# Kernel tuning notes

Measured on AMD Instinct MI355X. Metric: run time of the kernel, lower is better.

## Reference

```python
import jax, jax.numpy as jnp
import numpy as np

IN_SIZE = 768
FC_SIZE = 3072
H = 12
ATT = IN_SIZE // H
EPS = 1e-5


def setup_inputs() -> dict:
    key = jax.random.key(0)
    ks = jax.random.split(key, 12)
    B, S = 4, 1024
    x = jax.random.normal(ks[0], (B, S, IN_SIZE), dtype=jnp.float32)
    mask = jax.random.randint(ks[1], (B, S, S), 0, 2, dtype=jnp.int32)
    s = 1.0 / np.sqrt(IN_SIZE)
    WQ = jax.random.normal(ks[2], (IN_SIZE, IN_SIZE), dtype=jnp.float32) * s
    WK = jax.random.normal(ks[3], (IN_SIZE, IN_SIZE), dtype=jnp.float32) * s
    WV = jax.random.normal(ks[4], (IN_SIZE, IN_SIZE), dtype=jnp.float32) * s
    Wfc = jax.random.normal(ks[5], (IN_SIZE, IN_SIZE), dtype=jnp.float32) * s
    W1 = jax.random.normal(ks[6], (IN_SIZE, FC_SIZE), dtype=jnp.float32) * s
    b1 = jnp.zeros((FC_SIZE,), dtype=jnp.float32)
    W2 = jax.random.normal(ks[7], (FC_SIZE, IN_SIZE), dtype=jnp.float32) / np.sqrt(FC_SIZE)
    b2 = jnp.zeros((IN_SIZE,), dtype=jnp.float32)
    g1 = jnp.ones((IN_SIZE,), dtype=jnp.float32)
    be1 = jnp.zeros((IN_SIZE,), dtype=jnp.float32)
    g2 = jnp.ones((IN_SIZE,), dtype=jnp.float32)
    be2 = jnp.zeros((IN_SIZE,), dtype=jnp.float32)
    return dict(x=x, mask=mask, WQ=WQ, WK=WK, WV=WV, Wfc=Wfc,
                W1=W1, b1=b1, W2=W2, b2=b2, g1=g1, be1=be1, g2=g2, be2=be2)


def _layernorm(x, g, b):
    mu = jnp.mean(x, axis=-1, keepdims=True)
    var = jnp.var(x, axis=-1, keepdims=True)
    return (x - mu) * jax.lax.rsqrt(var + EPS) * g + b


def reference(x, mask, WQ, WK, WV, Wfc, W1, b1, W2, b2, g1, be1, g2, be2):
    B, S, D = x.shape
    # NOTE: original code scales by sqrt(h), not sqrt(head_dim)
    scale = np.sqrt(H).astype(np.float32)
    Q = (x @ WQ).reshape(B, S, H, ATT).transpose(0, 2, 1, 3)  # [B,H,S,d]
    K = (x @ WK).reshape(B, S, H, ATT).transpose(0, 2, 1, 3)
    V = (x @ WV).reshape(B, S, H, ATT).transpose(0, 2, 1, 3)
    alpha = jnp.einsum('bhqd,bhkd->bhqk', Q, K) / scale
    alpha = jnp.where(mask[:, None, :, :] == 0, -1e9, alpha)
    alpha = jax.nn.softmax(alpha, axis=-1)
    att = jnp.einsum('bhqk,bhkd->bhqd', alpha, V)
    att = att.transpose(0, 2, 1, 3).reshape(B, S, D)
    att = att @ Wfc
    norm_att = _layernorm(att + x, g1, be1)
    lin = jax.nn.relu(norm_att @ W1 + b1) @ W2 + b2
    out = _layernorm(lin + norm_att, g2, be2)
    return out
```

## Files before the change

### kernel.cpp

```cpp
#include <hip/hip_runtime.h>
#include <stdint.h>

#define DMODEL 768
#define DFC    3072
#define NHEAD  12
#define DHEAD  64
#define BSZ    4
#define SEQ    1024
#define NTOK   (BSZ*SEQ)
#define QKVN   (3*DMODEL)

typedef unsigned short u16;
typedef unsigned int   u32;
typedef unsigned long long u64;
typedef __bf16 bf16_t;
typedef bf16_t bf16x8 __attribute__((ext_vector_type(8)));
typedef float  f32x4  __attribute__((ext_vector_type(4)));

__device__ __forceinline__ u16 f2b(float f) {
  u32 u = __builtin_bit_cast(u32, f);
  u = (u + 0x7FFFu + ((u >> 16) & 1u)) >> 16;
  return (u16)u;
}

__device__ __forceinline__ void gload_lds16(const void* g, void* l) {
  __builtin_amdgcn_global_load_lds(
      (const __attribute__((address_space(1))) void*)g,
      (__attribute__((address_space(3))) void*)l, 16, 0, 0);
}


__global__ __launch_bounds__(256) void cast_f32_bf16(const float* __restrict__ in,
                                                     u16* __restrict__ out, int n4) {
  int i = blockIdx.x * 256 + threadIdx.x;
  if (i >= n4) return;
  float4 v = ((const float4*)in)[i];
  ushort4 o;
  o.x = f2b(v.x); o.y = f2b(v.y); o.z = f2b(v.z); o.w = f2b(v.w);
  ((ushort4*)out)[i] = o;
}

__global__ __launch_bounds__(256) void transpose_cast(const float* __restrict__ in,
                                                      u16* __restrict__ out, int K, int N) {
  __shared__ float tile[32][33];
  int bx = blockIdx.x * 32;
  int by = blockIdx.y * 32;
  int tx = threadIdx.x, ty = threadIdx.y;
#pragma unroll
  for (int i = 0; i < 4; ++i)
    tile[ty + i*8][tx] = in[(size_t)(by + ty + i*8) * N + bx + tx];
  __syncthreads();
#pragma unroll
  for (int i = 0; i < 4; ++i)
    out[(size_t)(bx + ty + i*8) * K + by + tx] = f2b(tile[tx][ty + i*8]);
}

__global__ __launch_bounds__(256) void pack_mask(const int* __restrict__ mask,
                                                 u64* __restrict__ mp) {
  int w = threadIdx.x >> 6, lane = threadIdx.x & 63;
  int idx = blockIdx.x * 4 + w;
  u64 bal = __ballot(mask[(size_t)idx * 64 + lane] != 0);
  if (lane == 0) mp[idx] = bal;
}

__global__ __launch_bounds__(256) void build_vt(const u16* __restrict__ QKVM,
                                                u16* __restrict__ VT) {
  __shared__ u16 t[64][72];
  int st = blockIdx.x, h = blockIdx.y, b = blockIdx.z;
  int tid = threadIdx.x;
  const u16* src = QKVM + ((size_t)(b * SEQ + st * 64)) * QKVN + 2 * DMODEL + h * DHEAD;
#pragma unroll
  for (int p = 0; p < 2; ++p) {
    int s = (p * 256 + tid) >> 3, c8 = tid & 7;
    *(uint4*)&t[s][c8 * 8] = *(const uint4*)&src[(size_t)s * QKVN + c8 * 8];
  }
  __syncthreads();
  u16* dst = VT + ((size_t)(b * NHEAD + h) * 64) * SEQ + st * 64;
#pragma unroll
  for (int p = 0; p < 2; ++p) {
    int d = (p * 256 + tid) >> 3, s8 = tid & 7;
    union { uint4 v; u16 s[8]; } o;
#pragma unroll
    for (int j = 0; j < 8; ++j) o.s[j] = t[s8 * 8 + j][d];
    *(uint4*)&dst[(size_t)d * SEQ + s8 * 8] = o.v;
  }
}

template <int MODE>
__global__ __launch_bounds__(256) void gemm_bt(const u16* __restrict__ A,
                                               const u16* __restrict__ Bt,
                                               void* __restrict__ Cout,
                                               const float* __restrict__ bias,
                                               int M, int N, int K) {
  __shared__ __align__(16) u16 ldsA[2][128 * 32];
  __shared__ __align__(16) u16 ldsB[2][128 * 32];
  int tid = threadIdx.x;
  int lane = tid & 63, l15 = lane & 15, g = lane >> 4;
  int w = tid >> 6, wm = w >> 1, wn = w & 1;
  int m0 = blockIdx.y * 128, n0 = blockIdx.x * 128;
  int NT = K >> 5;

  f32x4 acc[4][4];
#pragma unroll
  for (int i = 0; i < 4; ++i)
#pragma unroll
    for (int j = 0; j < 4; ++j) acc[i][j] = (f32x4){0.f, 0.f, 0.f, 0.f};

  const u16* gabase = A + (size_t)m0 * K;
  const u16* gbbase = Bt + (size_t)n0 * K;
  int wbase = tid & ~63;

  auto stage = [&](int kt, int buf) {
#pragma unroll
    for (int p = 0; p < 2; ++p) {
      int c = p * 256 + tid;
      int row = c >> 2, slot = c & 3;
      size_t goff = (size_t)row * K + kt * 32 + slot * 8;
      gload_lds16(gabase + goff, &ldsA[buf][(p * 256 + wbase) * 8]);
      gload_lds16(gbbase + goff, &ldsB[buf][(p * 256 + wbase) * 8]);
    }
  };

  stage(0, 0);
  __syncthreads();
  for (int kt = 0; kt < NT; ++kt) {
    int cur = kt & 1;
    if (kt + 1 < NT) stage(kt + 1, cur ^ 1);
    bf16x8 af[4], bfr[4];
#pragma unroll
    for (int i = 0; i < 4; ++i) {
      af[i]  = *(const bf16x8*)&ldsA[cur][(wm * 64 + i * 16 + l15) * 32 + g * 8];
      bfr[i] = *(const bf16x8*)&ldsB[cur][(wn * 64 + i * 16 + l15) * 32 + g * 8];
    }
#pragma unroll
    for (int i = 0; i < 4; ++i)
#pragma unroll
      for (int j = 0; j < 4; ++j)
        acc[i][j] = __builtin_amdgcn_mfma_f32_16x16x32_bf16(af[i], bfr[j], acc[i][j], 0, 0, 0);
    __syncthreads();
  }

#pragma unroll
  for (int i = 0; i < 4; ++i) {
#pragma unroll
    for (int j = 0; j < 4; ++j) {
#pragma unroll
      for (int r = 0; r < 4; ++r) {
        int row = m0 + wm * 64 + i * 16 + g * 4 + r;
        int col = n0 + wn * 64 + j * 16 + l15;
        float v = acc[i][j][r];
        if (MODE == 2 || MODE == 3) v += bias[col];
        if (MODE == 2) v = v > 0.f ? v : 0.f;
        if (MODE == 0 || MODE == 2)
          ((u16*)Cout)[(size_t)row * N + col] = f2b(v);
        else
          ((float*)Cout)[(size_t)row * N + col] = v;
      }
    }
  }
}

__global__ __launch_bounds__(256) void attn_kernel(const u16* __restrict__ QKVM,
                                                   const u16* __restrict__ VT,
                                                   const u64* __restrict__ MP,
                                                   u16* __restrict__ Om) {
  __shared__ __align__(16) u16 ldsK[2][64 * 64];
  __shared__ __align__(16) u16 ldsV[2][64 * 64];
  __shared__ __align__(16) u16 P_lds[4][16][72];

  int qt = blockIdx.x, h = blockIdx.y, b = blockIdx.z;
  int tid = threadIdx.x, w = tid >> 6, lane = tid & 63;
  int l15 = lane & 15, g = lane >> 4, l7 = lane & 7;
  int q0 = qt * 64 + w * 16;

  const u16* Qb = QKVM + (size_t)(b * SEQ) * QKVN + h * DHEAD;
  const u16* Kb = QKVM + (size_t)(b * SEQ) * QKVN + DMODEL + h * DHEAD;
  const u16* Vb = VT + (size_t)(b * NHEAD + h) * 64 * SEQ;

  bf16x8 qf[2];
  qf[0] = *(const bf16x8*)&Qb[(size_t)(q0 + l15) * QKVN + g * 8];
  qf[1] = *(const bf16x8*)&Qb[(size_t)(q0 + l15) * QKVN + 32 + g * 8];

  int r8 = lane >> 3, sl = lane & 7, slg = sl ^ r8;

  auto stage = [&](int kt, int buf) {
#pragma unroll
    for (int p = 0; p < 2; ++p) {
      int c = p * 4 + w;
      int row = c * 8 + r8;
      gload_lds16(Kb + (size_t)(kt * 64 + row) * QKVN + slg * 8, &ldsK[buf][c * 512]);
      gload_lds16(Vb + (size_t)row * SEQ + kt * 64 + slg * 8, &ldsV[buf][c * 512]);
    }
  };

  f32x4 acc[4];
  float ps[4];
#pragma unroll
  for (int d = 0; d < 4; ++d) acc[d] = (f32x4){0.f, 0.f, 0.f, 0.f};
#pragma unroll
  for (int r = 0; r < 4; ++r) ps[r] = 0.f;

  const float SC2 = 0.41650835f;

  stage(0, 0);
  __syncthreads();

  for (int kt = 0; kt < SEQ / 64; ++kt) {
    int cur = kt & 1;
    if (kt + 1 < SEQ / 64) stage(kt + 1, cur ^ 1);

    u64 mw[4];
#pragma unroll
    for (int r = 0; r < 4; ++r)
      mw[r] = MP[((size_t)(b * SEQ + q0 + g * 4 + r) << 4) | kt];

    f32x4 s[4];
#pragma unroll
    for (int fn = 0; fn < 4; ++fn) s[fn] = (f32x4){0.f, 0.f, 0.f, 0.f};
#pragma unroll
    for (int kf = 0; kf < 2; ++kf)
#pragma unroll
      for (int fn = 0; fn < 4; ++fn) {
        bf16x8 kfrag = *(const bf16x8*)((const char*)&ldsK[cur][0] +
                         (fn * 16 + l15) * 128 + (((kf * 4 + g) ^ l7) << 4));
        s[fn] = __builtin_amdgcn_mfma_f32_16x16x32_bf16(qf[kf], kfrag, s[fn], 0, 0, 0);
      }

#pragma unroll
    for (int fn = 0; fn < 4; ++fn) {
      u32 half0 = (fn & 2) ? (u32)(mw[0] >> 32) : (u32)mw[0];
      u32 half1 = (fn & 2) ? (u32)(mw[1] >> 32) : (u32)mw[1];
      u32 half2 = (fn & 2) ? (u32)(mw[2] >> 32) : (u32)mw[2];
      u32 half3 = (fn & 2) ? (u32)(mw[3] >> 32) : (u32)mw[3];
      u32 bitpos = ((fn & 1) << 4) + l15;
      u32 hv[4] = {half0, half1, half2, half3};
#pragma unroll
      for (int r = 0; r < 4; ++r) {
        float pe = __builtin_amdgcn_exp2f(s[fn][r] * SC2);
        float p = ((hv[r] >> bitpos) & 1u) ? pe : 0.f;
        ps[r] += p;
        P_lds[w][g * 4 + r][fn * 16 + l15] = f2b(p);
      }
    }

#pragma unroll
    for (int kf2 = 0; kf2 < 2; ++kf2) {
      bf16x8 pf = *(const bf16x8*)((const char*)&P_lds[w][0][0] +
                    l15 * 144 + (kf2 * 32 + g * 8) * 2);
#pragma unroll
      for (int d = 0; d < 4; ++d) {
        bf16x8 vf = *(const bf16x8*)((const char*)&ldsV[cur][0] +
                      (d * 16 + l15) * 128 + (((kf2 * 4 + g) ^ l7) << 4));
        acc[d] = __builtin_amdgcn_mfma_f32_16x16x32_bf16(pf, vf, acc[d], 0, 0, 0);
      }
    }
    __syncthreads();
  }

#pragma unroll
  for (int r = 0; r < 4; ++r) {
#pragma unroll
    for (int off = 1; off < 16; off <<= 1) ps[r] += __shfl_xor(ps[r], off);
    ps[r] = 1.f / ps[r];
  }
#pragma unroll
  for (int d = 0; d < 4; ++d)
#pragma unroll
    for (int r = 0; r < 4; ++r) {
      float o = acc[d][r] * ps[r];
      Om[(size_t)(b * SEQ + q0 + g * 4 + r) * DMODEL + h * DHEAD + d * 16 + l15] = f2b(o);
    }
}

template <bool WRITE_B16>
__global__ __launch_bounds__(256) void ln_res(const float* __restrict__ a,
                                              const float* __restrict__ res,
                                              const float* __restrict__ gam,
                                              const float* __restrict__ bet,
                                              float* __restrict__ of,
                                              u16* __restrict__ ob) {
  int w = threadIdx.x >> 6, lane = threadIdx.x & 63;
  int row = blockIdx.x * 4 + w;
  const float* pa = a + (size_t)row * DMODEL;
  const float* pr = res + (size_t)row * DMODEL;
  float v[12];
  float s = 0.f, s2 = 0.f;
#pragma unroll
  for (int j = 0; j < 12; ++j) {
    float x = pa[lane + j * 64] + pr[lane + j * 64];
    v[j] = x; s += x; s2 += x * x;
  }
#pragma unroll
  for (int off = 32; off; off >>= 1) {
    s += __shfl_xor(s, off);
    s2 += __shfl_xor(s2, off);
  }
  float mu = s * (1.f / DMODEL);
  float var = s2 * (1.f / DMODEL) - mu * mu;
  float rs = rsqrtf(var + 1e-5f);
#pragma unroll
  for (int j = 0; j < 12; ++j) {
    int c = lane + j * 64;
    float o = (v[j] - mu) * rs * gam[c] + bet[c];
    of[(size_t)row * DMODEL + c] = o;
    if (WRITE_B16) ob[(size_t)row * DMODEL + c] = f2b(o);
  }
}

extern "C" void kernel_launch(void* const* d_in, const int* in_sizes, int n_in,
                              void* d_out, int out_size, void* d_ws, size_t ws_size,
                              hipStream_t stream) {
  const float* x   = (const float*)d_in[0];
  const int*   msk = (const int*)d_in[1];
  const float* WQ  = (const float*)d_in[2];
  const float* WK  = (const float*)d_in[3];
  const float* WV  = (const float*)d_in[4];
  const float* Wfc = (const float*)d_in[5];
  const float* W1  = (const float*)d_in[6];
  const float* b1  = (const float*)d_in[7];
  const float* W2  = (const float*)d_in[8];
  const float* b2  = (const float*)d_in[9];
  const float* g1  = (const float*)d_in[10];
  const float* be1 = (const float*)d_in[11];
  const float* g2  = (const float*)d_in[12];
  const float* be2 = (const float*)d_in[13];
  float* out = (float*)d_out;

  char* ws = (char*)d_ws;
  size_t off = 0;
  auto alloc = [&](size_t bytes) {
    void* p = ws + off;
    off += (bytes + 255) & ~(size_t)255;
    return p;
  };
  u16* XB    = (u16*)alloc((size_t)NTOK * DMODEL * 2);
  u16* WQKVT = (u16*)alloc((size_t)QKVN * DMODEL * 2);
  u16* WFCT  = (u16*)alloc((size_t)DMODEL * DMODEL * 2);
  u16* W1T   = (u16*)alloc((size_t)DMODEL * DFC * 2);
  u16* W2T   = (u16*)alloc((size_t)DFC * DMODEL * 2);
  u16* QKVM  = (u16*)alloc((size_t)NTOK * QKVN * 2);
  u16* VT    = (u16*)alloc((size_t)NTOK * DMODEL * 2);
  u64* MP    = (u64*)alloc((size_t)BSZ * SEQ * (SEQ / 64) * 8);
  float* ATTP = (float*)alloc((size_t)NTOK * DMODEL * 4);
  float* NAF  = (float*)alloc((size_t)NTOK * DMODEL * 4);
  u16*  NAB   = (u16*)alloc((size_t)NTOK * DMODEL * 2);
  u16*  ATTO = XB;
  u16*  HMID = QKVM;
  float* LIN = ATTP;

  cast_f32_bf16<<<dim3((NTOK * DMODEL) / 4 / 256), dim3(256), 0, stream>>>(x, XB, (NTOK * DMODEL) / 4);
  transpose_cast<<<dim3(DMODEL / 32, DMODEL / 32), dim3(32, 8), 0, stream>>>(WQ, WQKVT, DMODEL, DMODEL);
  transpose_cast<<<dim3(DMODEL / 32, DMODEL / 32), dim3(32, 8), 0, stream>>>(WK, WQKVT + (size_t)DMODEL * DMODEL, DMODEL, DMODEL);
  transpose_cast<<<dim3(DMODEL / 32, DMODEL / 32), dim3(32, 8), 0, stream>>>(WV, WQKVT + (size_t)2 * DMODEL * DMODEL, DMODEL, DMODEL);
  transpose_cast<<<dim3(DMODEL / 32, DMODEL / 32), dim3(32, 8), 0, stream>>>(Wfc, WFCT, DMODEL, DMODEL);
  transpose_cast<<<dim3(DFC / 32, DMODEL / 32), dim3(32, 8), 0, stream>>>(W1, W1T, DMODEL, DFC);
  transpose_cast<<<dim3(DMODEL / 32, DFC / 32), dim3(32, 8), 0, stream>>>(W2, W2T, DFC, DMODEL);
  pack_mask<<<dim3(BSZ * SEQ * (SEQ / 64) / 4), dim3(256), 0, stream>>>(msk, MP);

  gemm_bt<0><<<dim3(QKVN / 128, NTOK / 128), dim3(256), 0, stream>>>(XB, WQKVT, QKVM, nullptr, NTOK, QKVN, DMODEL);
  build_vt<<<dim3(SEQ / 64, NHEAD, BSZ), dim3(256), 0, stream>>>(QKVM, VT);
  attn_kernel<<<dim3(SEQ / 64, NHEAD, BSZ), dim3(256), 0, stream>>>(QKVM, VT, MP, ATTO);

  gemm_bt<1><<<dim3(DMODEL / 128, NTOK / 128), dim3(256), 0, stream>>>(ATTO, WFCT, ATTP, nullptr, NTOK, DMODEL, DMODEL);
  ln_res<true><<<dim3(NTOK / 4), dim3(256), 0, stream>>>(ATTP, x, g1, be1, NAF, NAB);
  gemm_bt<2><<<dim3(DFC / 128, NTOK / 128), dim3(256), 0, stream>>>(NAB, W1T, HMID, b1, NTOK, DFC, DMODEL);
  gemm_bt<3><<<dim3(DMODEL / 128, NTOK / 128), dim3(256), 0, stream>>>(HMID, W2T, LIN, b2, NTOK, DMODEL, DFC);
  ln_res<false><<<dim3(NTOK / 4), dim3(256), 0, stream>>>(LIN, NAF, g2, be2, out, nullptr);

  (void)in_sizes; (void)n_in; (void)out_size; (void)ws_size;
}
```

Baseline: 327.9 us.

## Split-K the N=768 GEMMs with atomics and swizzle GEMM LDS layout

The two GEMMs with N=768 (output projection and second FFN matmul) now use split-K across blockIdx.z (2 and 4 ways) and accumulate into memset-zeroed fp32 buffers with atomicAdd. The b2 bias add moves into the final layernorm. The GEMM LDS staging and fragment reads get an XOR swizzle on the 16-byte slot to cut bank conflicts. Buffers are reassigned to fixed workspace offsets, and the fp32 accumulators alias QKVM and XB. The aim is more blocks for the small-grid GEMMs, at the cost of two memsets, atomic traffic, and a non-deterministic summation order.

```diff
diff --git a/kernel.cpp b/kernel.cpp
--- a/kernel.cpp
+++ b/kernel.cpp
@@ -86,7 +86,7 @@
   }
 }
 
-template <int MODE>
+template <int MODE, int SPLIT>
 __global__ __launch_bounds__(256) void gemm_bt(const u16* __restrict__ A,
                                                const u16* __restrict__ Bt,
                                                void* __restrict__ Cout,
@@ -98,7 +98,9 @@
   int lane = tid & 63, l15 = lane & 15, g = lane >> 4;
   int w = tid >> 6, wm = w >> 1, wn = w & 1;
   int m0 = blockIdx.y * 128, n0 = blockIdx.x * 128;
-  int NT = K >> 5;
+  int KS = K / SPLIT;
+  int k0 = blockIdx.z * KS;
+  int NT = KS >> 5;
 
   f32x4 acc[4][4];
 #pragma unroll
@@ -106,20 +108,23 @@
 #pragma unroll
     for (int j = 0; j < 4; ++j) acc[i][j] = (f32x4){0.f, 0.f, 0.f, 0.f};
 
-  const u16* gabase = A + (size_t)m0 * K;
-  const u16* gbbase = Bt + (size_t)n0 * K;
+  const u16* gabase = A + (size_t)m0 * K + k0;
+  const u16* gbbase = Bt + (size_t)n0 * K + k0;
   int wbase = tid & ~63;
+  int lswz = (lane & 3) ^ ((lane >> 3) & 3);
 
   auto stage = [&](int kt, int buf) {
 #pragma unroll
     for (int p = 0; p < 2; ++p) {
       int c = p * 256 + tid;
-      int row = c >> 2, slot = c & 3;
-      size_t goff = (size_t)row * K + kt * 32 + slot * 8;
+      int row = c >> 2;
+      size_t goff = (size_t)row * K + kt * 32 + lswz * 8;
       gload_lds16(gabase + goff, &ldsA[buf][(p * 256 + wbase) * 8]);
       gload_lds16(gbbase + goff, &ldsB[buf][(p * 256 + wbase) * 8]);
     }
   };
+
+  int rswz = (l15 >> 1) & 3;
 
   stage(0, 0);
   __syncthreads();
@@ -129,8 +134,8 @@
     bf16x8 af[4], bfr[4];
 #pragma unroll
     for (int i = 0; i < 4; ++i) {
-      af[i]  = *(const bf16x8*)&ldsA[cur][(wm * 64 + i * 16 + l15) * 32 + g * 8];
-      bfr[i] = *(const bf16x8*)&ldsB[cur][(wn * 64 + i * 16 + l15) * 32 + g * 8];
+      af[i]  = *(const bf16x8*)&ldsA[cur][(wm * 64 + i * 16 + l15) * 32 + (g ^ rswz) * 8];
+      bfr[i] = *(const bf16x8*)&ldsB[cur][(wn * 64 + i * 16 + l15) * 32 + (g ^ rswz) * 8];
     }
 #pragma unroll
     for (int i = 0; i < 4; ++i)
@@ -149,12 +154,14 @@
         int row = m0 + wm * 64 + i * 16 + g * 4 + r;
         int col = n0 + wn * 64 + j * 16 + l15;
         float v = acc[i][j][r];
-        if (MODE == 2 || MODE == 3) v += bias[col];
-        if (MODE == 2) v = v > 0.f ? v : 0.f;
-        if (MODE == 0 || MODE == 2)
+        if (MODE == 2) {
+          v += bias[col];
+          v = v > 0.f ? v : 0.f;
+        }
+        if (MODE == 4)
+          atomicAdd(&((float*)Cout)[(size_t)row * N + col], v);
+        else
           ((u16*)Cout)[(size_t)row * N + col] = f2b(v);
-        else
-          ((float*)Cout)[(size_t)row * N + col] = v;
       }
     }
   }
@@ -228,12 +235,11 @@
 
 #pragma unroll
     for (int fn = 0; fn < 4; ++fn) {
-      u32 half0 = (fn & 2) ? (u32)(mw[0] >> 32) : (u32)mw[0];
-      u32 half1 = (fn & 2) ? (u32)(mw[1] >> 32) : (u32)mw[1];
-      u32 half2 = (fn & 2) ? (u32)(mw[2] >> 32) : (u32)mw[2];
-      u32 half3 = (fn & 2) ? (u32)(mw[3] >> 32) : (u32)mw[3];
+      u32 hv[4];
+#pragma unroll
+      for (int r = 0; r < 4; ++r)
+        hv[r] = (fn & 2) ? (u32)(mw[r] >> 32) : (u32)mw[r];
       u32 bitpos = ((fn & 1) << 4) + l15;
-      u32 hv[4] = {half0, half1, half2, half3};
 #pragma unroll
       for (int r = 0; r < 4; ++r) {
         float pe = __builtin_amdgcn_exp2f(s[fn][r] * SC2);
@@ -272,9 +278,10 @@
     }
 }
 
-template <bool WRITE_B16>
+template <bool WRITE_B16, bool ADDB>
 __global__ __launch_bounds__(256) void ln_res(const float* __restrict__ a,
                                               const float* __restrict__ res,
+                                              const float* __restrict__ badd,
                                               const float* __restrict__ gam,
                                               const float* __restrict__ bet,
                                               float* __restrict__ of,
@@ -287,7 +294,9 @@
   float s = 0.f, s2 = 0.f;
 #pragma unroll
   for (int j = 0; j < 12; ++j) {
-    float x = pa[lane + j * 64] + pr[lane + j * 64];
+    int c = lane + j * 64;
+    float x = pa[c] + pr[c];
+    if (ADDB) x += badd[c];
     v[j] = x; s += x; s2 += x * x;
   }
 #pragma unroll
@@ -327,26 +336,20 @@
   float* out = (float*)d_out;
 
   char* ws = (char*)d_ws;
-  size_t off = 0;
-  auto alloc = [&](size_t bytes) {
-    void* p = ws + off;
-    off += (bytes + 255) & ~(size_t)255;
-    return p;
-  };
-  u16* XB    = (u16*)alloc((size_t)NTOK * DMODEL * 2);
-  u16* WQKVT = (u16*)alloc((size_t)QKVN * DMODEL * 2);
-  u16* WFCT  = (u16*)alloc((size_t)DMODEL * DMODEL * 2);
-  u16* W1T   = (u16*)alloc((size_t)DMODEL * DFC * 2);
-  u16* W2T   = (u16*)alloc((size_t)DFC * DMODEL * 2);
-  u16* QKVM  = (u16*)alloc((size_t)NTOK * QKVN * 2);
-  u16* VT    = (u16*)alloc((size_t)NTOK * DMODEL * 2);
-  u64* MP    = (u64*)alloc((size_t)BSZ * SEQ * (SEQ / 64) * 8);
-  float* ATTP = (float*)alloc((size_t)NTOK * DMODEL * 4);
-  float* NAF  = (float*)alloc((size_t)NTOK * DMODEL * 4);
-  u16*  NAB   = (u16*)alloc((size_t)NTOK * DMODEL * 2);
-  u16*  ATTO = XB;
-  u16*  HMID = QKVM;
-  float* LIN = ATTP;
+  u16*  XB    = (u16*)(ws + 0);
+  u16*  WQKVT = (u16*)(ws + 6291456);
+  u16*  WFCT  = (u16*)(ws + 9830400);
+  u16*  W1T   = (u16*)(ws + 11010048);
+  u16*  W2T   = (u16*)(ws + 15728640);
+  u16*  QKVM  = (u16*)(ws + 20447232);
+  u16*  VT    = (u16*)(ws + 39321600);
+  u64*  MP    = (u64*)(ws + 45613056);
+  float* NAF  = (float*)(ws + 46137344);
+  u16*  NAB   = (u16*)(ws + 58720256);
+  u16*   ATTO    = XB;
+  float* PROJACC = (float*)QKVM;
+  u16*   HMID    = QKVM;
+  float* LINACC  = (float*)ws;
 
   cast_f32_bf16<<<dim3((NTOK * DMODEL) / 4 / 256), dim3(256), 0, stream>>>(x, XB, (NTOK * DMODEL) / 4);
   transpose_cast<<<dim3(DMODEL / 32, DMODEL / 32), dim3(32, 8), 0, stream>>>(WQ, WQKVT, DMODEL, DMODEL);
@@ -357,15 +360,18 @@
   transpose_cast<<<dim3(DMODEL / 32, DFC / 32), dim3(32, 8), 0, stream>>>(W2, W2T, DFC, DMODEL);
   pack_mask<<<dim3(BSZ * SEQ * (SEQ / 64) / 4), dim3(256), 0, stream>>>(msk, MP);
 
-  gemm_bt<0><<<dim3(QKVN / 128, NTOK / 128), dim3(256), 0, stream>>>(XB, WQKVT, QKVM, nullptr, NTOK, QKVN, DMODEL);
+  gemm_bt<0, 1><<<dim3(QKVN / 128, NTOK / 128, 1), dim3(256), 0, stream>>>(XB, WQKVT, QKVM, nullptr, NTOK, QKVN, DMODEL);
   build_vt<<<dim3(SEQ / 64, NHEAD, BSZ), dim3(256), 0, stream>>>(QKVM, VT);
   attn_kernel<<<dim3(SEQ / 64, NHEAD, BSZ), dim3(256), 0, stream>>>(QKVM, VT, MP, ATTO);
 
-  gemm_bt<1><<<dim3(DMODEL / 128, NTOK / 128), dim3(256), 0, stream>>>(ATTO, WFCT, ATTP, nullptr, NTOK, DMODEL, DMODEL);
-  ln_res<true><<<dim3(NTOK / 4), dim3(256), 0, stream>>>(ATTP, x, g1, be1, NAF, NAB);
-  gemm_bt<2><<<dim3(DFC / 128, NTOK / 128), dim3(256), 0, stream>>>(NAB, W1T, HMID, b1, NTOK, DFC, DMODEL);
-  gemm_bt<3><<<dim3(DMODEL / 128, NTOK / 128), dim3(256), 0, stream>>>(HMID, W2T, LIN, b2, NTOK, DMODEL, DFC);
-  ln_res<false><<<dim3(NTOK / 4), dim3(256), 0, stream>>>(LIN, NAF, g2, be2, out, nullptr);
+  hipMemsetAsync(PROJACC, 0, (size_t)NTOK * DMODEL * 4, stream);
+  gemm_bt<4, 2><<<dim3(DMODEL / 128, NTOK / 128, 2), dim3(256), 0, stream>>>(ATTO, WFCT, PROJACC, nullptr, NTOK, DMODEL, DMODEL);
+  ln_res<true, false><<<dim3(NTOK / 4), dim3(256), 0, stream>>>(PROJACC, x, nullptr, g1, be1, NAF, NAB);
+
+  gemm_bt<2, 1><<<dim3(DFC / 128, NTOK / 128, 1), dim3(256), 0, stream>>>(NAB, W1T, HMID, b1, NTOK, DFC, DMODEL);
+  hipMemsetAsync(LINACC, 0, (size_t)NTOK * DMODEL * 4, stream);
+  gemm_bt<4, 4><<<dim3(DMODEL / 128, NTOK / 128, 4), dim3(256), 0, stream>>>(HMID, W2T, LINACC, nullptr, NTOK, DMODEL, DFC);
+  ln_res<false, true><<<dim3(NTOK / 4), dim3(256), 0, stream>>>(LINACC, NAF, b2, g2, be2, out, nullptr);
 
   (void)in_sizes; (void)n_in; (void)out_size; (void)ws_size;
 }
```

New measurement: 342.5 us. 1.04x slower.
